# Kernel tuning notes

Measured on AMD Instinct MI355X. Metric: run time of the kernel, lower is better.

Reference implementation:

```python
import jax, jax.numpy as jnp
import numpy as np

N_NODES = 100000
N_EDGES = 1600000


def _sage_conv(x, src, dst, W_neigh, W_self, b, n_nodes):
    # mean aggregation over in-neighbors (dst receives from src), DGL 'mean' SAGEConv
    agg = jax.ops.segment_sum(x[src], dst, num_segments=n_nodes)          # [N, d]
    deg = jax.ops.segment_sum(jnp.ones((src.shape[0],), x.dtype), dst,
                              num_segments=n_nodes)                        # [N]
    mean = agg / jnp.maximum(deg, 1.0)[:, None]
    return x @ W_self + mean @ W_neigh + b


def setup_inputs() -> dict:
    key = jax.random.key(0)
    ks = jax.random.split(key, 10)
    d_in, d_hid, d_out = 64, 64, 32
    x = jax.random.normal(ks[0], (N_NODES, d_in), jnp.float32)
    src = jax.random.randint(ks[1], (N_EDGES,), 0, N_NODES, jnp.int32)
    dst = jax.random.randint(ks[2], (N_EDGES,), 0, N_NODES, jnp.int32)
    def w(k, i, o):
        return jax.random.normal(k, (i, o), jnp.float32) / np.sqrt(i)
    return {
        "x": x, "src": src, "dst": dst,
        "W_self1": w(ks[3], d_in, d_hid), "W_neigh1": w(ks[4], d_in, d_hid),
        "b1": jnp.zeros((d_hid,), jnp.float32),
        "W_self2": w(ks[5], d_hid, d_hid), "W_neigh2": w(ks[6], d_hid, d_hid),
        "b2": jnp.zeros((d_hid,), jnp.float32),
        "W_self3": w(ks[7], d_hid, d_out), "W_neigh3": w(ks[8], d_hid, d_out),
        "b3": jnp.zeros((d_out,), jnp.float32),
    }


def reference(x, src, dst, W_self1, W_neigh1, b1, W_self2, W_neigh2, b2,
              W_self3, W_neigh3, b3):
    n = x.shape[0]
    h = _sage_conv(x, src, dst, W_neigh1, W_self1, b1, n)
    h = _sage_conv(h, src, dst, W_neigh2, W_self2, b2, n)
    h = _sage_conv(h, src, dst, W_neigh3, W_self3, b3, n)
    h = jax.nn.relu(h)
    # Dropout(0.5) treated in eval mode (identity) for deterministic reference
    return h
```

## Files before the change

kernel.cpp:

```cpp
#include <hip/hip_runtime.h>


#define NN 100000
#define NE 1600000
#define GBLOCKS 1024


__global__ __launch_bounds__(256) void deg_count_kernel(
    const int* __restrict__ dst, int* __restrict__ deg, int n_edges) {
  int e = blockIdx.x * 256 + threadIdx.x;
  if (e < n_edges) atomicAdd(&deg[dst[e]], 1);
}

__global__ __launch_bounds__(256) void scan_partial_kernel(
    const int* __restrict__ deg, int* __restrict__ partials, int n_nodes) {
  __shared__ int sb[256];
  int t = threadIdx.x;
  int i = blockIdx.x * 256 + t;
  sb[t] = (i < n_nodes) ? deg[i] : 0;
  __syncthreads();
  for (int off = 128; off > 0; off >>= 1) {
    if (t < off) sb[t] += sb[t + off];
    __syncthreads();
  }
  if (t == 0) partials[blockIdx.x] = sb[0];
}

__global__ __launch_bounds__(512) void scan_top_kernel(
    int* __restrict__ partials, int nb, int* __restrict__ rowp, int n_nodes) {
  __shared__ int tmp[512];
  int t = threadIdx.x;
  int v = (t < nb) ? partials[t] : 0;
  tmp[t] = v;
  __syncthreads();
  for (int off = 1; off < 512; off <<= 1) {
    int add = (t >= off) ? tmp[t - off] : 0;
    __syncthreads();
    tmp[t] += add;
    __syncthreads();
  }
  if (t < nb) partials[t] = tmp[t] - v;
  if (t == 511) rowp[n_nodes] = tmp[511];
}

__global__ __launch_bounds__(256) void scan_final_kernel(
    const int* __restrict__ deg, const int* __restrict__ partials,
    int* __restrict__ rowp, int* __restrict__ cursor,
    float* __restrict__ degf, int n_nodes) {
  __shared__ int tmp[256];
  int t = threadIdx.x;
  int i = blockIdx.x * 256 + t;
  int v = (i < n_nodes) ? deg[i] : 0;
  tmp[t] = v;
  __syncthreads();
  for (int off = 1; off < 256; off <<= 1) {
    int add = (t >= off) ? tmp[t - off] : 0;
    __syncthreads();
    tmp[t] += add;
    __syncthreads();
  }
  if (i < n_nodes) {
    int exc = tmp[t] - v + partials[blockIdx.x];
    rowp[i] = exc;
    cursor[i] = exc;
    degf[i] = fmaxf((float)v, 1.0f);
  }
}

__global__ __launch_bounds__(256) void fill_kernel(
    const int* __restrict__ src, const int* __restrict__ dst,
    int* __restrict__ cursor, int* __restrict__ col, int n_edges) {
  int e = blockIdx.x * 256 + threadIdx.x;
  if (e < n_edges) {
    int pos = atomicAdd(&cursor[dst[e]], 1);
    col[pos] = src[e];
  }
}


template <int DOUT, bool RELU>
__global__ __launch_bounds__(256) void sage_layer_kernel(
    const float* __restrict__ h_in,
    const int* __restrict__ rowp,
    const int* __restrict__ col,
    const float* __restrict__ degf,
    const float* __restrict__ Wself,
    const float* __restrict__ Wneigh,
    const float* __restrict__ bias,
    float* __restrict__ h_out) {
  __shared__ float Wt[DOUT][132];
  __shared__ float rowbuf[4][128];
  __shared__ int   idxbuf[4][64];

  const int tid  = threadIdx.x;
  const int wave = tid >> 6;
  const int lane = tid & 63;

  for (int idx = tid; idx < DOUT * 128; idx += 256) {
    int c = idx & (DOUT - 1);
    int k = idx / DOUT;
    Wt[c][k] = (k < 64) ? Wself[k * DOUT + c] : Wneigh[(k - 64) * DOUT + c];
  }
  __syncthreads();

  const float bval = (lane < DOUT) ? bias[lane] : 0.0f;

  for (int g = blockIdx.x; g < NN / 4; g += GBLOCKS) {
    const int   un   = __builtin_amdgcn_readfirstlane(g * 4 + wave);
    const int   e0   = rowp[un];
    const int   e1   = rowp[un + 1];
    const float self = h_in[un * 64 + lane];

    float acc = 0.0f;
    for (int base = e0; base < e1; base += 64) {
      idxbuf[wave][lane] = (base + lane < e1) ? col[base + lane] : 0;
      const int m = min(64, e1 - base);
      for (int j = 0; j < m; j += 8) {
        const int4 q0 = *(const int4*)&idxbuf[wave][j];
        const int4 q1 = *(const int4*)&idxbuf[wave][j + 4];
        const float* p0 = h_in + __builtin_amdgcn_readfirstlane(q0.x) * 64;
        const float* p1 = h_in + __builtin_amdgcn_readfirstlane(q0.y) * 64;
        const float* p2 = h_in + __builtin_amdgcn_readfirstlane(q0.z) * 64;
        const float* p3 = h_in + __builtin_amdgcn_readfirstlane(q0.w) * 64;
        const float* p4 = h_in + __builtin_amdgcn_readfirstlane(q1.x) * 64;
        const float* p5 = h_in + __builtin_amdgcn_readfirstlane(q1.y) * 64;
        const float* p6 = h_in + __builtin_amdgcn_readfirstlane(q1.z) * 64;
        const float* p7 = h_in + __builtin_amdgcn_readfirstlane(q1.w) * 64;
        float a0 = p0[lane];
        float a1 = p1[lane];
        float a2 = p2[lane];
        float a3 = p3[lane];
        float a4 = p4[lane];
        float a5 = p5[lane];
        float a6 = p6[lane];
        float a7 = p7[lane];
        a0 = (j + 0 < m) ? a0 : 0.0f;
        a1 = (j + 1 < m) ? a1 : 0.0f;
        a2 = (j + 2 < m) ? a2 : 0.0f;
        a3 = (j + 3 < m) ? a3 : 0.0f;
        a4 = (j + 4 < m) ? a4 : 0.0f;
        a5 = (j + 5 < m) ? a5 : 0.0f;
        a6 = (j + 6 < m) ? a6 : 0.0f;
        a7 = (j + 7 < m) ? a7 : 0.0f;
        acc += ((a0 + a1) + (a2 + a3)) + ((a4 + a5) + (a6 + a7));
      }
    }

    rowbuf[wave][lane]      = self;
    rowbuf[wave][64 + lane] = acc / degf[un];

    if (lane < DOUT) {
      float o0 = 0.f, o1 = 0.f, o2 = 0.f, o3 = 0.f;
#pragma unroll
      for (int j = 0; j < 32; ++j) {
        const float4 w = *(const float4*)&Wt[lane][j * 4];
        const float4 r = *(const float4*)&rowbuf[wave][j * 4];
        o0 = fmaf(r.x, w.x, o0);
        o1 = fmaf(r.y, w.y, o1);
        o2 = fmaf(r.z, w.z, o2);
        o3 = fmaf(r.w, w.w, o3);
      }
      float o = ((o0 + o1) + (o2 + o3)) + bval;
      if (RELU) o = fmaxf(o, 0.0f);
      h_out[un * DOUT + lane] = o;
    }
  }
}


extern "C" void kernel_launch(void* const* d_in, const int* in_sizes, int n_in,
                              void* d_out, int out_size, void* d_ws, size_t ws_size,
                              hipStream_t stream) {
  const float* x   = (const float*)d_in[0];
  const int*   src = (const int*)d_in[1];
  const int*   dst = (const int*)d_in[2];
  const float* Ws1 = (const float*)d_in[3];
  const float* Wn1 = (const float*)d_in[4];
  const float* b1  = (const float*)d_in[5];
  const float* Ws2 = (const float*)d_in[6];
  const float* Wn2 = (const float*)d_in[7];
  const float* b2  = (const float*)d_in[8];
  const float* Ws3 = (const float*)d_in[9];
  const float* Wn3 = (const float*)d_in[10];
  const float* b3  = (const float*)d_in[11];
  float* out = (float*)d_out;

  char* ws = (char*)d_ws;
  size_t off = 0;
  auto take = [&](size_t bytes) -> void* {
    void* p = ws + off;
    off += (bytes + 255) & ~(size_t)255;
    return p;
  };
  int*   deg      = (int*)take((size_t)NN * 4);
  float* degf     = (float*)take((size_t)NN * 4);
  int*   rowp     = (int*)take((size_t)(NN + 1) * 4);
  int*   cursor   = (int*)take((size_t)NN * 4);
  int*   partials = (int*)take(1024 * 4);
  int*   col      = (int*)take((size_t)NE * 4);
  float* h1       = (float*)take((size_t)NN * 64 * 4);
  float* h2       = (float*)take((size_t)NN * 64 * 4);
  (void)ws_size; (void)in_sizes; (void)n_in; (void)out_size;

  hipMemsetAsync(deg, 0, (size_t)NN * 4, stream);

  const int EB = (NE + 255) / 256;
  const int NB = (NN + 255) / 256;

  deg_count_kernel<<<EB, 256, 0, stream>>>(dst, deg, NE);
  scan_partial_kernel<<<NB, 256, 0, stream>>>(deg, partials, NN);
  scan_top_kernel<<<1, 512, 0, stream>>>(partials, NB, rowp, NN);
  scan_final_kernel<<<NB, 256, 0, stream>>>(deg, partials, rowp, cursor, degf, NN);
  fill_kernel<<<EB, 256, 0, stream>>>(src, dst, cursor, col, NE);

  sage_layer_kernel<64, false><<<GBLOCKS, 256, 0, stream>>>(x,  rowp, col, degf, Ws1, Wn1, b1, h1);
  sage_layer_kernel<64, false><<<GBLOCKS, 256, 0, stream>>>(h1, rowp, col, degf, Ws2, Wn2, b2, h2);
  sage_layer_kernel<32, true ><<<GBLOCKS, 256, 0, stream>>>(h2, rowp, col, degf, Ws3, Wn3, b3, out);
}
```

Measured before the change: 642.3 us.

## Split SAGE layer into node-parallel mean aggregation and separate GEMM kernels

Each layer's fused gather-and-project kernel becomes two kernels. A new aggregation kernel maps 16 lanes per node, each lane gathering float4 slices, so one wave handles four nodes at once, and it writes the neighbour mean to a workspace buffer. A separate GEMM kernel then reads the self row and the mean row and applies the weights. This aims to raise gather parallelism and memory-level concurrency, at the cost of an extra round trip of the mean buffer through global memory and extra kernel launches.

```diff
diff --git a/kernel.cpp b/kernel.cpp
--- a/kernel.cpp
+++ b/kernel.cpp
@@ -3,7 +3,7 @@
 
 #define NN 100000
 #define NE 1600000
-#define GBLOCKS 1024
+#define GEMM_BLOCKS 1024
 
 
 __global__ __launch_bounds__(256) void deg_count_kernel(
@@ -78,19 +78,75 @@
 }
 
 
-template <int DOUT, bool RELU>
-__global__ __launch_bounds__(256) void sage_layer_kernel(
+__global__ __launch_bounds__(256) void agg_mean_kernel(
     const float* __restrict__ h_in,
     const int* __restrict__ rowp,
     const int* __restrict__ col,
     const float* __restrict__ degf,
+    float* __restrict__ mean_out) {
+  const int tid  = threadIdx.x;
+  const int wave = tid >> 6;
+  const int lane = tid & 63;
+  const int g    = lane >> 4;
+  const int f4   = (lane & 15) * 4;
+
+  const int n = blockIdx.x * 16 + wave * 4 + g;
+
+  const int e0 = rowp[n];
+  const int e1 = rowp[n + 1];
+  const int ecount = e1 - e0;
+
+  float4 acc = {0.f, 0.f, 0.f, 0.f};
+  int e = 0;
+  for (; e + 8 <= ecount; e += 8) {
+    int i0 = col[e0 + e + 0], i1 = col[e0 + e + 1];
+    int i2 = col[e0 + e + 2], i3 = col[e0 + e + 3];
+    int i4 = col[e0 + e + 4], i5 = col[e0 + e + 5];
+    int i6 = col[e0 + e + 6], i7 = col[e0 + e + 7];
+    float4 v0 = *(const float4*)(h_in + (size_t)i0 * 64 + f4);
+    float4 v1 = *(const float4*)(h_in + (size_t)i1 * 64 + f4);
+    float4 v2 = *(const float4*)(h_in + (size_t)i2 * 64 + f4);
+    float4 v3 = *(const float4*)(h_in + (size_t)i3 * 64 + f4);
+    float4 v4 = *(const float4*)(h_in + (size_t)i4 * 64 + f4);
+    float4 v5 = *(const float4*)(h_in + (size_t)i5 * 64 + f4);
+    float4 v6 = *(const float4*)(h_in + (size_t)i6 * 64 + f4);
+    float4 v7 = *(const float4*)(h_in + (size_t)i7 * 64 + f4);
+    acc.x += ((v0.x + v1.x) + (v2.x + v3.x)) + ((v4.x + v5.x) + (v6.x + v7.x));
+    acc.y += ((v0.y + v1.y) + (v2.y + v3.y)) + ((v4.y + v5.y) + (v6.y + v7.y));
+    acc.z += ((v0.z + v1.z) + (v2.z + v3.z)) + ((v4.z + v5.z) + (v6.z + v7.z));
+    acc.w += ((v0.w + v1.w) + (v2.w + v3.w)) + ((v4.w + v5.w) + (v6.w + v7.w));
+  }
+  if (e < ecount) {
+    const int last = e1 - 1;
+#pragma unroll
+    for (int u = 0; u < 8; ++u) {
+      int ee = e0 + e + u;
+      int ii = col[ee <= last ? ee : last];
+      float4 v = *(const float4*)(h_in + (size_t)ii * 64 + f4);
+      float msk = (e + u < ecount) ? 1.0f : 0.0f;
+      acc.x = fmaf(v.x, msk, acc.x);
+      acc.y = fmaf(v.y, msk, acc.y);
+      acc.z = fmaf(v.z, msk, acc.z);
+      acc.w = fmaf(v.w, msk, acc.w);
+    }
+  }
+
+  const float d = degf[n];
+  float4 mv = {acc.x / d, acc.y / d, acc.z / d, acc.w / d};
+  *(float4*)(mean_out + (size_t)n * 64 + f4) = mv;
+}
+
+
+template <int DOUT, bool RELU>
+__global__ __launch_bounds__(256) void gemm_kernel(
+    const float* __restrict__ h_self,
+    const float* __restrict__ mean,
     const float* __restrict__ Wself,
     const float* __restrict__ Wneigh,
     const float* __restrict__ bias,
     float* __restrict__ h_out) {
   __shared__ float Wt[DOUT][132];
   __shared__ float rowbuf[4][128];
-  __shared__ int   idxbuf[4][64];
 
   const int tid  = threadIdx.x;
   const int wave = tid >> 6;
@@ -105,49 +161,10 @@
 
   const float bval = (lane < DOUT) ? bias[lane] : 0.0f;
 
-  for (int g = blockIdx.x; g < NN / 4; g += GBLOCKS) {
-    const int   un   = __builtin_amdgcn_readfirstlane(g * 4 + wave);
-    const int   e0   = rowp[un];
-    const int   e1   = rowp[un + 1];
-    const float self = h_in[un * 64 + lane];
-
-    float acc = 0.0f;
-    for (int base = e0; base < e1; base += 64) {
-      idxbuf[wave][lane] = (base + lane < e1) ? col[base + lane] : 0;
-      const int m = min(64, e1 - base);
-      for (int j = 0; j < m; j += 8) {
-        const int4 q0 = *(const int4*)&idxbuf[wave][j];
-        const int4 q1 = *(const int4*)&idxbuf[wave][j + 4];
-        const float* p0 = h_in + __builtin_amdgcn_readfirstlane(q0.x) * 64;
-        const float* p1 = h_in + __builtin_amdgcn_readfirstlane(q0.y) * 64;
-        const float* p2 = h_in + __builtin_amdgcn_readfirstlane(q0.z) * 64;
-        const float* p3 = h_in + __builtin_amdgcn_readfirstlane(q0.w) * 64;
-        const float* p4 = h_in + __builtin_amdgcn_readfirstlane(q1.x) * 64;
-        const float* p5 = h_in + __builtin_amdgcn_readfirstlane(q1.y) * 64;
-        const float* p6 = h_in + __builtin_amdgcn_readfirstlane(q1.z) * 64;
-        const float* p7 = h_in + __builtin_amdgcn_readfirstlane(q1.w) * 64;
-        float a0 = p0[lane];
-        float a1 = p1[lane];
-        float a2 = p2[lane];
-        float a3 = p3[lane];
-        float a4 = p4[lane];
-        float a5 = p5[lane];
-        float a6 = p6[lane];
-        float a7 = p7[lane];
-        a0 = (j + 0 < m) ? a0 : 0.0f;
-        a1 = (j + 1 < m) ? a1 : 0.0f;
-        a2 = (j + 2 < m) ? a2 : 0.0f;
-        a3 = (j + 3 < m) ? a3 : 0.0f;
-        a4 = (j + 4 < m) ? a4 : 0.0f;
-        a5 = (j + 5 < m) ? a5 : 0.0f;
-        a6 = (j + 6 < m) ? a6 : 0.0f;
-        a7 = (j + 7 < m) ? a7 : 0.0f;
-        acc += ((a0 + a1) + (a2 + a3)) + ((a4 + a5) + (a6 + a7));
-      }
-    }
-
-    rowbuf[wave][lane]      = self;
-    rowbuf[wave][64 + lane] = acc / degf[un];
+  for (int gblk = blockIdx.x; gblk < NN / 4; gblk += GEMM_BLOCKS) {
+    const int n = gblk * 4 + wave;
+    rowbuf[wave][lane]      = h_self[(size_t)n * 64 + lane];
+    rowbuf[wave][64 + lane] = mean[(size_t)n * 64 + lane];
 
     if (lane < DOUT) {
       float o0 = 0.f, o1 = 0.f, o2 = 0.f, o3 = 0.f;
@@ -162,7 +179,7 @@
       }
       float o = ((o0 + o1) + (o2 + o3)) + bval;
       if (RELU) o = fmaxf(o, 0.0f);
-      h_out[un * DOUT + lane] = o;
+      h_out[(size_t)n * DOUT + lane] = o;
     }
   }
 }
@@ -200,12 +217,14 @@
   int*   col      = (int*)take((size_t)NE * 4);
   float* h1       = (float*)take((size_t)NN * 64 * 4);
   float* h2       = (float*)take((size_t)NN * 64 * 4);
+  float* meanbuf  = (float*)take((size_t)NN * 64 * 4);
   (void)ws_size; (void)in_sizes; (void)n_in; (void)out_size;
 
   hipMemsetAsync(deg, 0, (size_t)NN * 4, stream);
 
   const int EB = (NE + 255) / 256;
   const int NB = (NN + 255) / 256;
+  const int AB = NN / 16;
 
   deg_count_kernel<<<EB, 256, 0, stream>>>(dst, deg, NE);
   scan_partial_kernel<<<NB, 256, 0, stream>>>(deg, partials, NN);
@@ -213,7 +232,12 @@
   scan_final_kernel<<<NB, 256, 0, stream>>>(deg, partials, rowp, cursor, degf, NN);
   fill_kernel<<<EB, 256, 0, stream>>>(src, dst, cursor, col, NE);
 
-  sage_layer_kernel<64, false><<<GBLOCKS, 256, 0, stream>>>(x,  rowp, col, degf, Ws1, Wn1, b1, h1);
-  sage_layer_kernel<64, false><<<GBLOCKS, 256, 0, stream>>>(h1, rowp, col, degf, Ws2, Wn2, b2, h2);
-  sage_layer_kernel<32, true ><<<GBLOCKS, 256, 0, stream>>>(h2, rowp, col, degf, Ws3, Wn3, b3, out);
-}
+  agg_mean_kernel<<<AB, 256, 0, stream>>>(x, rowp, col, degf, meanbuf);
+  gemm_kernel<64, false><<<GEMM_BLOCKS, 256, 0, stream>>>(x, meanbuf, Ws1, Wn1, b1, h1);
+
+  agg_mean_kernel<<<AB, 256, 0, stream>>>(h1, rowp, col, degf, meanbuf);
+  gemm_kernel<64, false><<<GEMM_BLOCKS, 256, 0, stream>>>(h1, meanbuf, Ws2, Wn2, b2, h2);
+
+  agg_mean_kernel<<<AB, 256, 0, stream>>>(h2, rowp, col, degf, meanbuf);
+  gemm_kernel<32, true ><<<GEMM_BLOCKS, 256, 0, stream>>>(h2, meanbuf, Ws3, Wn3, b3, out);
+}
```

New measurement: 619.9 us. 1.04x faster.
